# Optimization experiments

Hardware: AMD Instinct MI355X
Metric: run time of the kernel (lower is better)

## Reference

```python
import jax, jax.numpy as jnp
import numpy as np

D_MODEL = 256
NUM_HEADS = 8
D_HEAD = D_MODEL // NUM_HEADS


def setup_inputs() -> dict:
    key = jax.random.key(0)
    ks = jax.random.split(key, 12)
    B, N, M, C = 1, 512, 512, D_MODEL
    s = 1.0 / np.sqrt(C)
    inp = {
        'input_q': jax.random.normal(ks[0], (B, N, C), jnp.float32),
        'input_k': jax.random.normal(ks[1], (B, M, C), jnp.float32),
        'input_v': jax.random.normal(ks[2], (B, M, C), jnp.float32),
        'embed_qk': jax.random.normal(ks[3], (B, N, M, C), jnp.float32),
        'Wq': jax.random.normal(ks[4], (C, C), jnp.float32) * s,
        'bq': jnp.zeros((C,), jnp.float32),
        'Wk': jax.random.normal(ks[5], (C, C), jnp.float32) * s,
        'bk': jnp.zeros((C,), jnp.float32),
        'Wv': jax.random.normal(ks[6], (C, C), jnp.float32) * s,
        'bv': jnp.zeros((C,), jnp.float32),
        'Wp': jax.random.normal(ks[7], (C, C), jnp.float32) * s,
        'bp': jnp.zeros((C,), jnp.float32),
    }
    return inp


def _split_heads(x, h):
    # (b, n, h*c) -> (b, h, n, c)
    b, n, _ = x.shape
    return x.reshape(b, n, h, -1).transpose(0, 2, 1, 3)


def reference(input_q, input_k, input_v, embed_qk, Wq, bq, Wk, bk, Wv, bv, Wp, bp):
    H = NUM_HEADS
    q = _split_heads(input_q @ Wq.T + bq, H)            # (b,h,n,c)
    k = _split_heads(input_k @ Wk.T + bk, H)            # (b,h,m,c)
    v = _split_heads(input_v @ Wv.T + bv, H)            # (b,h,m,c)
    p = embed_qk @ Wp.T + bp                            # (b,n,m,h*c)
    b_, n_, m_, _ = p.shape
    p = p.reshape(b_, n_, m_, H, -1).transpose(0, 3, 1, 2, 4)  # (b,h,n,m,c)
    scores_p = jnp.einsum('bhnc,bhnmc->bhnm', q, p)
    scores_e = jnp.einsum('bhnc,bhmc->bhnm', q, k)
    scores = (scores_e + scores_p) / jnp.sqrt(jnp.float32(D_HEAD))
    attn = jax.nn.softmax(scores, axis=-1)              # (b,h,n,m)
    hidden = jnp.einsum('bhnm,bhmc->bhnc', attn, v)
    b2, h2, n2, c2 = hidden.shape
    hidden = hidden.transpose(0, 2, 1, 3).reshape(b2, n2, h2 * c2)  # (b,n,C)
    return hidden, attn
```

## Files before the change

### kernel.cpp

```cpp
#include <hip/hip_runtime.h>
#include <math.h>

#define NN 512
#define CC 256
#define HH 8
#define DH 32

typedef float vf4 __attribute__((ext_vector_type(4)));

__global__ __launch_bounds__(256) void proj_kernel(
    const float* __restrict__ xq, const float* __restrict__ xk, const float* __restrict__ xv,
    const float* __restrict__ Wq, const float* __restrict__ bq,
    const float* __restrict__ Wk, const float* __restrict__ bk,
    const float* __restrict__ Wv, const float* __restrict__ bv,
    const float* __restrict__ Wp, const float* __restrict__ bp,
    float* __restrict__ qf, float* __restrict__ kf, float* __restrict__ vf,
    float* __restrict__ qw, float* __restrict__ qbp)
{
    __shared__ float x_lds[3][CC];
    __shared__ float q_lds[CC];
    const int t = threadIdx.x;
    const int n = blockIdx.x;

    if (t < 192) {
        int X = t >> 6, c4 = (t & 63) * 4;
        const float* xs = (X == 0) ? xq : (X == 1) ? xk : xv;
        *reinterpret_cast<float4*>(&x_lds[X][c4]) =
            *reinterpret_cast<const float4*>(xs + (size_t)n * CC + c4);
    }
    __syncthreads();

    const int j = t;
    {
        float accq = 0.f, acck = 0.f, accv = 0.f;
        const float* wq = Wq + (size_t)j * CC;
        const float* wk = Wk + (size_t)j * CC;
        const float* wv = Wv + (size_t)j * CC;
        #pragma unroll 4
        for (int k4 = 0; k4 < CC / 4; ++k4) {
            float4 a = *reinterpret_cast<const float4*>(wq + k4 * 4);
            float4 b = *reinterpret_cast<const float4*>(wk + k4 * 4);
            float4 d = *reinterpret_cast<const float4*>(wv + k4 * 4);
            const float* x0 = &x_lds[0][k4 * 4];
            const float* x1 = &x_lds[1][k4 * 4];
            const float* x2 = &x_lds[2][k4 * 4];
            accq += x0[0]*a.x + x0[1]*a.y + x0[2]*a.z + x0[3]*a.w;
            acck += x1[0]*b.x + x1[1]*b.y + x1[2]*b.z + x1[3]*b.w;
            accv += x2[0]*d.x + x2[1]*d.y + x2[2]*d.z + x2[3]*d.w;
        }
        float vq = accq + bq[j];
        kf[(size_t)n * CC + j] = acck + bk[j];
        vf[(size_t)n * CC + j] = accv + bv[j];
        qf[(size_t)n * CC + j] = vq;
        q_lds[j] = vq;
    }
    __syncthreads();

    {
        const int jq = t & 63;
        const int hp = t >> 6;
        const int h0 = 2 * hp, h1 = h0 + 1;
        float4 a0 = {0.f, 0.f, 0.f, 0.f}, a1 = {0.f, 0.f, 0.f, 0.f};
        #pragma unroll
        for (int cc = 0; cc < DH; ++cc) {
            float q0 = q_lds[h0 * DH + cc];
            float q1 = q_lds[h1 * DH + cc];
            float4 w0 = *reinterpret_cast<const float4*>(Wp + (size_t)(h0 * DH + cc) * CC + jq * 4);
            float4 w1 = *reinterpret_cast<const float4*>(Wp + (size_t)(h1 * DH + cc) * CC + jq * 4);
            a0.x += q0 * w0.x; a0.y += q0 * w0.y; a0.z += q0 * w0.z; a0.w += q0 * w0.w;
            a1.x += q1 * w1.x; a1.y += q1 * w1.y; a1.z += q1 * w1.z; a1.w += q1 * w1.w;
        }
        *reinterpret_cast<float4*>(qw + ((size_t)n * HH + h0) * CC + jq * 4) = a0;
        *reinterpret_cast<float4*>(qw + ((size_t)n * HH + h1) * CC + jq * 4) = a1;
    }
    if (t < HH) {
        float s = 0.f;
        for (int cc = 0; cc < DH; ++cc) s += q_lds[t * DH + cc] * bp[t * DH + cc];
        qbp[(size_t)n * HH + t] = s;
    }
}

__global__ __launch_bounds__(256) void escore_kernel(
    const float* __restrict__ qf, const float* __restrict__ kf, float* __restrict__ esc)
{
    const int b = blockIdx.x;
    const int h = b >> 6, nt = (b >> 3) & 7, mt = b & 7;
    const int n0 = nt * 64, m0 = mt * 64;
    const int t = threadIdx.x;

    __shared__ float q_t[64][33];
    __shared__ float k_t[64][33];

    #pragma unroll
    for (int it = 0; it < 2; ++it) {
        int idx = t + it * 256;
        int row = idx >> 3, c4 = (idx & 7) * 4;
        float4 qv = *reinterpret_cast<const float4*>(qf + (size_t)(n0 + row) * CC + h * DH + c4);
        float4 kv = *reinterpret_cast<const float4*>(kf + (size_t)(m0 + row) * CC + h * DH + c4);
        q_t[row][c4] = qv.x; q_t[row][c4+1] = qv.y; q_t[row][c4+2] = qv.z; q_t[row][c4+3] = qv.w;
        k_t[row][c4] = kv.x; k_t[row][c4+1] = kv.y; k_t[row][c4+2] = kv.z; k_t[row][c4+3] = kv.w;
    }
    __syncthreads();

    const int tx = t & 15, ty = t >> 4;
    float acc[4][4];
    #pragma unroll
    for (int i = 0; i < 4; ++i)
        #pragma unroll
        for (int jq = 0; jq < 4; ++jq) acc[i][jq] = 0.f;

    for (int cc = 0; cc < DH; ++cc) {
        float qa[4], kb[4];
        #pragma unroll
        for (int i = 0; i < 4; ++i) qa[i] = q_t[ty * 4 + i][cc];
        #pragma unroll
        for (int jq = 0; jq < 4; ++jq) kb[jq] = k_t[tx * 4 + jq][cc];
        #pragma unroll
        for (int i = 0; i < 4; ++i)
            #pragma unroll
            for (int jq = 0; jq < 4; ++jq) acc[i][jq] += qa[i] * kb[jq];
    }

    #pragma unroll
    for (int i = 0; i < 4; ++i) {
        float4 v = {acc[i][0], acc[i][1], acc[i][2], acc[i][3]};
        *reinterpret_cast<float4*>(
            esc + ((size_t)(n0 + ty * 4 + i) * HH + h) * NN + m0 + tx * 4) = v;
    }
}

__device__ __forceinline__ float reduce8(const float a[HH], int c) {
    const bool b1 = (c & 1), b2 = (c & 2), b4 = (c & 4);
    float t0 = b1 ? a[0] : a[4], t1 = b1 ? a[1] : a[5],
          t2 = b1 ? a[2] : a[6], t3 = b1 ? a[3] : a[7];
    float r0 = (b1 ? a[4] : a[0]) + __shfl_xor(t0, 1);
    float r1 = (b1 ? a[5] : a[1]) + __shfl_xor(t1, 1);
    float r2 = (b1 ? a[6] : a[2]) + __shfl_xor(t2, 1);
    float r3 = (b1 ? a[7] : a[3]) + __shfl_xor(t3, 1);
    t0 = b2 ? r0 : r2; t1 = b2 ? r1 : r3;
    float s0 = (b2 ? r2 : r0) + __shfl_xor(t0, 2);
    float s1 = (b2 ? r3 : r1) + __shfl_xor(t1, 2);
    t0 = b4 ? s0 : s1;
    float u0 = (b4 ? s1 : s0) + __shfl_xor(t0, 4);
    u0 += __shfl_xor(u0, 8);
    return u0;
}

__global__ __launch_bounds__(256) void estream_kernel(
    const float* __restrict__ E, const float* __restrict__ qw,
    float* __restrict__ scores)
{
    const int b = blockIdx.x;
    const int n = b >> 3, slab = b & 7;
    const int m0 = slab * 64;
    const int t = threadIdx.x;
    const int v = t >> 6, l = t & 63;
    const int r = l >> 4, c = l & 15;

    __shared__ float qw_lds[HH][CC];
    __shared__ float s_out[HH][68];

    {
        const float4* src = reinterpret_cast<const float4*>(qw + (size_t)n * HH * CC);
        reinterpret_cast<float4*>(qw_lds)[t] = src[t];
        reinterpret_cast<float4*>(qw_lds)[t + 256] = src[t + 256];
    }
    __syncthreads();

    const int mrow = m0 + v * 16 + r;

    float acc[4][HH];
    #pragma unroll
    for (int it = 0; it < 4; ++it)
        #pragma unroll
        for (int h = 0; h < HH; ++h) acc[it][h] = 0.f;

    const float* Ebase = E + ((size_t)n * NN) * CC;
    #pragma unroll
    for (int co = 0; co < 4; ++co) {
        const int o = co * 64 + c * 4;
        vf4 e4[4];
        #pragma unroll
        for (int it = 0; it < 4; ++it)
            e4[it] = __builtin_nontemporal_load(reinterpret_cast<const vf4*>(
                Ebase + (size_t)(mrow + it * 4) * CC + o));
        #pragma unroll
        for (int h = 0; h < HH; ++h) {
            float4 wv = *reinterpret_cast<const float4*>(&qw_lds[h][o]);
            #pragma unroll
            for (int it = 0; it < 4; ++it)
                acc[it][h] += e4[it][0]*wv.x + e4[it][1]*wv.y +
                              e4[it][2]*wv.z + e4[it][3]*wv.w;
        }
    }

    #pragma unroll
    for (int it = 0; it < 4; ++it) {
        float u0 = reduce8(acc[it], c);
        if (!(c & 8)) {
            int h = (c & 1) * 4 + (c & 2) + ((c >> 2) & 1);
            s_out[h][v * 16 + it * 4 + r] = u0;
        }
    }
    __syncthreads();

    {
        int h0 = t >> 6, row = t & 63;
        scores[((size_t)n * HH + h0) * NN + m0 + row] = s_out[h0][row];
        int h1 = h0 + 4;
        scores[((size_t)n * HH + h1) * NN + m0 + row] = s_out[h1][row];
    }
}

__global__ __launch_bounds__(512) void softmax_hidden_kernel(
    const float* __restrict__ esc, const float* __restrict__ scores,
    const float* __restrict__ qbp, const float* __restrict__ vf,
    float* __restrict__ attn_out, float* __restrict__ out_hidden)
{
    const int n = blockIdx.x;
    const int t = threadIdx.x;
    const int w = t >> 6, l = t & 63;

    __shared__ float s_lds[HH][NN + 4];
    __shared__ float part_lds[HH][CC];

    {
        const int h = w;
        const float qb = qbp[(size_t)n * HH + h];
        const float scale = 0.17677669529663687f;
        const float* ep = esc    + ((size_t)n * HH + h) * NN;
        const float* sp = scores + ((size_t)n * HH + h) * NN;
        float vals[8];
        float mx = -1e30f;
        #pragma unroll
        for (int i = 0; i < 8; ++i) {
            vals[i] = (ep[l + i * 64] + sp[l + i * 64] + qb) * scale;
            mx = fmaxf(mx, vals[i]);
        }
        #pragma unroll
        for (int off = 32; off > 0; off >>= 1) mx = fmaxf(mx, __shfl_xor(mx, off));
        float sum = 0.f;
        #pragma unroll
        for (int i = 0; i < 8; ++i) { vals[i] = __expf(vals[i] - mx); sum += vals[i]; }
        #pragma unroll
        for (int off = 32; off > 0; off >>= 1) sum += __shfl_xor(sum, off);
        float inv = 1.0f / sum;
        #pragma unroll
        for (int i = 0; i < 8; ++i) {
            float p = vals[i] * inv;
            int m = l + i * 64;
            s_lds[h][m] = p;
            __builtin_nontemporal_store(p, attn_out + ((size_t)h * NN + n) * NN + m);
        }
    }
    __syncthreads();

    {
        const int quad = t & 63;
        const int slice = w;
        const int h = quad >> 3;
        float4 a4 = {0.f, 0.f, 0.f, 0.f};
        const float* vb = vf + quad * 4;
        for (int mm = 0; mm < 64; ++mm) {
            int m = slice * 64 + mm;
            float a = s_lds[h][m];
            float4 vv = *reinterpret_cast<const float4*>(vb + (size_t)m * CC);
            a4.x += a * vv.x; a4.y += a * vv.y; a4.z += a * vv.z; a4.w += a * vv.w;
        }
        *reinterpret_cast<float4*>(&part_lds[slice][quad * 4]) = a4;
    }
    __syncthreads();
    if (t < 256) {
        float s = 0.f;
        #pragma unroll
        for (int sl = 0; sl < 8; ++sl) s += part_lds[sl][t];
        out_hidden[(size_t)n * CC + t] = s;
    }
}

extern "C" void kernel_launch(void* const* d_in, const int* in_sizes, int n_in,
                              void* d_out, int out_size, void* d_ws, size_t ws_size,
                              hipStream_t stream) {
    const float* xq = (const float*)d_in[0];
    const float* xk = (const float*)d_in[1];
    const float* xv = (const float*)d_in[2];
    const float* E  = (const float*)d_in[3];
    const float* Wq = (const float*)d_in[4];
    const float* bq = (const float*)d_in[5];
    const float* Wk = (const float*)d_in[6];
    const float* bk = (const float*)d_in[7];
    const float* Wv = (const float*)d_in[8];
    const float* bv = (const float*)d_in[9];
    const float* Wp = (const float*)d_in[10];
    const float* bp = (const float*)d_in[11];

    float* ws = (float*)d_ws;
    float* qf     = ws;
    float* kf     = qf + NN * CC;
    float* vf     = kf + NN * CC;
    float* qw     = vf + NN * CC;
    float* qbp    = qw + (size_t)NN * HH * CC;
    float* esc    = qbp + NN * HH;
    float* scores = esc + (size_t)NN * HH * NN;

    float* out_hidden = (float*)d_out;
    float* out_attn   = out_hidden + NN * CC;

    proj_kernel<<<NN, 256, 0, stream>>>(xq, xk, xv, Wq, bq, Wk, bk, Wv, bv, Wp, bp,
                                        qf, kf, vf, qw, qbp);
    escore_kernel<<<512, 256, 0, stream>>>(qf, kf, esc);
    estream_kernel<<<NN * 8, 256, 0, stream>>>(E, qw, scores);
    softmax_hidden_kernel<<<NN, 512, 0, stream>>>(esc, scores, qbp, vf,
                                                  out_attn, out_hidden);
}
```

Before: 127.6 us.

## Hold per-row qw weights in registers and map one warp to full E rows

The E-streaming kernel stops staging the per-query qw matrix in LDS. Each lane now keeps its 4-channel slice of all 8 heads in registers, and a wavefront covers a full 256-channel E row per load. This removes the LDS fill, its barrier and the repeated LDS reads, at the cost of two extra cross-lane shuffle reductions per row and a per-row reduction instead of a per-thread accumulation. Launch bounds now request 4 blocks per SM to raise occupancy.

Result: no change. 127.6 us (-0.0%).

```diff
diff --git a/kernel.cpp b/kernel.cpp
--- a/kernel.cpp
+++ b/kernel.cpp
@@ -146,7 +146,7 @@
     return u0;
 }
 
-__global__ __launch_bounds__(256) void estream_kernel(
+__global__ __launch_bounds__(256, 4) void estream_kernel(
     const float* __restrict__ E, const float* __restrict__ qw,
     float* __restrict__ scores)
 {
@@ -155,51 +155,39 @@
     const int m0 = slab * 64;
     const int t = threadIdx.x;
     const int v = t >> 6, l = t & 63;
-    const int r = l >> 4, c = l & 15;
-
-    __shared__ float qw_lds[HH][CC];
+    const int c = l & 15;
+
     __shared__ float s_out[HH][68];
 
-    {
-        const float4* src = reinterpret_cast<const float4*>(qw + (size_t)n * HH * CC);
-        reinterpret_cast<float4*>(qw_lds)[t] = src[t];
-        reinterpret_cast<float4*>(qw_lds)[t + 256] = src[t + 256];
-    }
-    __syncthreads();
-
-    const int mrow = m0 + v * 16 + r;
-
-    float acc[4][HH];
-    #pragma unroll
-    for (int it = 0; it < 4; ++it)
-        #pragma unroll
-        for (int h = 0; h < HH; ++h) acc[it][h] = 0.f;
-
-    const float* Ebase = E + ((size_t)n * NN) * CC;
-    #pragma unroll
-    for (int co = 0; co < 4; ++co) {
-        const int o = co * 64 + c * 4;
+    vf4 qwr[HH];
+    #pragma unroll
+    for (int h = 0; h < HH; ++h)
+        qwr[h] = *reinterpret_cast<const vf4*>(qw + ((size_t)n * HH + h) * CC + l * 4);
+
+    const float* Ebase = E + ((size_t)n * NN + m0 + v * 16) * CC;
+
+    #pragma unroll
+    for (int g = 0; g < 4; ++g) {
         vf4 e4[4];
         #pragma unroll
         for (int it = 0; it < 4; ++it)
             e4[it] = __builtin_nontemporal_load(reinterpret_cast<const vf4*>(
-                Ebase + (size_t)(mrow + it * 4) * CC + o));
-        #pragma unroll
-        for (int h = 0; h < HH; ++h) {
-            float4 wv = *reinterpret_cast<const float4*>(&qw_lds[h][o]);
+                Ebase + (size_t)(g * 4 + it) * CC + l * 4));
+
+        #pragma unroll
+        for (int it = 0; it < 4; ++it) {
+            float a[HH];
             #pragma unroll
-            for (int it = 0; it < 4; ++it)
-                acc[it][h] += e4[it][0]*wv.x + e4[it][1]*wv.y +
-                              e4[it][2]*wv.z + e4[it][3]*wv.w;
-        }
-    }
-
-    #pragma unroll
-    for (int it = 0; it < 4; ++it) {
-        float u0 = reduce8(acc[it], c);
-        if (!(c & 8)) {
-            int h = (c & 1) * 4 + (c & 2) + ((c >> 2) & 1);
-            s_out[h][v * 16 + it * 4 + r] = u0;
+            for (int h = 0; h < HH; ++h)
+                a[h] = e4[it][0]*qwr[h][0] + e4[it][1]*qwr[h][1] +
+                       e4[it][2]*qwr[h][2] + e4[it][3]*qwr[h][3];
+            float u0 = reduce8(a, c);
+            u0 += __shfl_xor(u0, 16);
+            u0 += __shfl_xor(u0, 32);
+            if (l < 8) {
+                int h = (c & 1) * 4 + (c & 2) + ((c >> 2) & 1);
+                s_out[h][v * 16 + g * 4 + it] = u0;
+            }
         }
     }
     __syncthreads();
```
